# Optimization experiments

Hardware: AMD Instinct MI355X
Metric: run time of the kernel (lower is better)

## Reference

```python
import jax, jax.numpy as jnp
import numpy as np
from jax import lax

B, H, V, L = 128, 256, 130, 100  # batch, hidden_size, vocab per stream, decode length


def _gru(x, h, wih, whh, bih, bhh):
    # torch.nn.GRUCell math
    gi = x @ wih.T + bih
    gh = h @ whh.T + bhh
    ir, iz, inn = jnp.split(gi, 3, axis=-1)
    hr, hz, hn = jnp.split(gh, 3, axis=-1)
    r = jax.nn.sigmoid(ir + hr)
    u = jax.nn.sigmoid(iz + hz)
    n = jnp.tanh(inn + r * hn)
    return (1.0 - u) * n + u * h


def _forward(z, gru1_wih, gru1_whh, gru1_bih, gru1_bhh,
             gru2_wih, gru2_whh, gru2_bih, gru2_bhh,
             ctx_wih, ctx_whh, ctx_bih, ctx_bhh,
             out_w, out_b, hid_w, hid_b, emb, length):
    b = z.shape[0]
    hidden = jnp.tanh(z @ hid_w.T + hid_b)                      # [B,H]
    h3 = jnp.broadcast_to(hidden[None], (3, b, hidden.shape[-1]))
    note0 = jnp.broadcast_to(emb[:, 0][:, None, :], (3, b, emb.shape[-1]))  # embed index 0
    vgru = jax.vmap(_gru)  # over the 3 parallel streams

    def step(carry, _):
        g1h, g2h, context, note = carry
        zb = jnp.broadcast_to(z[None], note.shape)
        g1h = vgru(jnp.concatenate([note, zb], -1), g1h,
                   gru1_wih, gru1_whh, gru1_bih, gru1_bhh)       # [3,B,H]
        unroll = g1h
        logits = []
        for i in range(3):  # fixed structural unroll (3 streams)
            ctx_in = jnp.concatenate([unroll[0], unroll[1], unroll[2]], -1)  # [B,3H]
            context = _gru(ctx_in, context, ctx_wih, ctx_whh, ctx_bih, ctx_bhh)
            h2 = _gru(jnp.concatenate([context, z], -1), g2h[i],
                      gru2_wih[i], gru2_whh[i], gru2_bih[i], gru2_bhh[i])
            g2h = g2h.at[i].set(h2)
            lg = (unroll[i] + h2) @ out_w[i].T + out_b[i]        # [B,V]
            logits.append(lg)
            ni = emb[i][jnp.argmax(lg, axis=-1)]                 # greedy sample -> embed
            note = note.at[i].set(ni)
            # NOTE: original code uses self.gru1[1] here (fixed index 1) -- kept faithful
            unroll = unroll.at[i].set(_gru(jnp.concatenate([ni, z], -1), unroll[i],
                                           gru1_wih[1], gru1_whh[1], gru1_bih[1], gru1_bhh[1]))
        return (g1h, g2h, context, note), jnp.stack(logits)     # [3,B,V]

    _, ys = lax.scan(step, (h3, h3, hidden, note0), None, length=length)
    return jnp.transpose(ys, (1, 2, 0, 3))                      # [3,B,L,V]


def setup_inputs() -> dict:
    key = jax.random.key(0)
    ks = jax.random.split(key, 18)
    s = 0.05
    n = lambda k, shp: jax.random.normal(k, shp, jnp.float32) * s
    return {
        "z": jax.random.normal(ks[0], (B, H), jnp.float32),
        "gru1_wih": n(ks[1], (3, 3 * H, 2 * H)),
        "gru1_whh": n(ks[2], (3, 3 * H, H)),
        "gru1_bih": n(ks[3], (3, 3 * H)),
        "gru1_bhh": n(ks[4], (3, 3 * H)),
        "gru2_wih": n(ks[5], (3, 3 * H, 2 * H)),
        "gru2_whh": n(ks[6], (3, 3 * H, H)),
        "gru2_bih": n(ks[7], (3, 3 * H)),
        "gru2_bhh": n(ks[8], (3, 3 * H)),
        "ctx_wih": n(ks[9], (3 * H, 3 * H)),
        "ctx_whh": n(ks[10], (3 * H, H)),
        "ctx_bih": n(ks[11], (3 * H,)),
        "ctx_bhh": n(ks[12], (3 * H,)),
        "out_w": n(ks[13], (3, V, H)),
        "out_b": n(ks[14], (3, V)),
        "hid_w": n(ks[15], (H, H)),
        "hid_b": n(ks[16], (H,)),
        "emb": n(ks[17], (3, V, H)),
        "length": L,
    }


def reference(z, gru1_wih, gru1_whh, gru1_bih, gru1_bhh,
              gru2_wih, gru2_whh, gru2_bih, gru2_bhh,
              ctx_wih, ctx_whh, ctx_bih, ctx_bhh,
              out_w, out_b, hid_w, hid_b, emb, length):
    return _forward(z, gru1_wih, gru1_whh, gru1_bih, gru1_bhh,
                    gru2_wih, gru2_whh, gru2_bih, gru2_bhh,
                    ctx_wih, ctx_whh, ctx_bih, ctx_bhh,
                    out_w, out_b, hid_w, hid_b, emb, length)
```

## Files before the change

### kernel.cpp

```cpp
#include <hip/hip_runtime.h>
#include <math.h>

#define B 128
#define H 256
#define V 130
#define L 100
#define G3 768
#define BH (B*H)
#define NWG 256
#define NT 1024

#define OFF_FLAGS 0
#define OFF_XRANK 512
#define OFF_CLAIM 640
#define OFF_HID   1024
#define OFF_Z1    (OFF_HID + BH)
#define OFF_Z2    (OFF_Z1 + 3*B*G3)
#define OFF_G1HA  (OFF_Z2 + 3*B*G3)
#define OFF_G1HB  (OFF_G1HA + 3*BH)
#define OFF_H2A   (OFF_G1HB + 3*BH)
#define OFF_H2B   (OFF_H2A + 3*BH)
#define OFF_CTXA  (OFF_H2B + 3*BH)
#define OFF_CTXB  (OFF_CTXA + BH)
#define OFF_U0    (OFF_CTXB + BH)
#define OFF_U1    (OFF_U0 + 3*BH)
#define OFF_NOTE  (OFF_U1 + 3*BH)

typedef float v4f __attribute__((ext_vector_type(4)));

__device__ __forceinline__ float sigmoidf_(float x) { return 1.0f / (1.0f + expf(-x)); }

__device__ __forceinline__ v4f load_coh4(const float* p) {
  v4f v;
  asm volatile("global_load_dwordx4 %0, %1, off sc0 sc1" : "=v"(v) : "v"(p) : "memory");
  return v;
}
__device__ __forceinline__ void store_coh(float* p, float v) {
  asm volatile("global_store_dword %0, %1, off sc0 sc1" :: "v"(p), "v"(v) : "memory");
}
__device__ __forceinline__ void store_coh4(float* p, v4f v) {
  asm volatile("global_store_dwordx4 %0, %1, off sc0 sc1" :: "v"(p), "v"(v) : "memory");
}
__device__ __forceinline__ void waitvm0() {
  asm volatile("s_waitcnt vmcnt(0)" ::: "memory");
}

__device__ __forceinline__ void group_barrier(int* cnt, int grp, int target, int tid) {
  waitvm0();
  __syncthreads();
  if (tid == 0) {
    int* c = cnt + grp * 16;
    __hip_atomic_fetch_add(c, 1, __ATOMIC_RELAXED, __HIP_MEMORY_SCOPE_AGENT);
    while (__hip_atomic_load(c, __ATOMIC_RELAXED, __HIP_MEMORY_SCOPE_AGENT) < target)
      __builtin_amdgcn_s_sleep(1);
  }
  __syncthreads();
}

template <int NCHUNK>
__device__ void gru_phase(
    const float* __restrict__ xc0, const float* __restrict__ xc1,
    const float* __restrict__ xc2, const float* __restrict__ xc3,
    const float* __restrict__ wih, int wih_stride,
    const float* __restrict__ whh,
    const float* __restrict__ zadd,
    const float* __restrict__ bih,
    const float* __restrict__ bhh,
    float* __restrict__ out0, float* __restrict__ out1,
    float* smem, int row0, int col0, int tid)
{
  const float* xc[4] = {xc0, xc1, xc2, xc3};
  v4f stg;
  int sc = 0, srr = 0, sk4 = 0;
  const int nldv = NCHUNK * 256;
  if (tid < nldv) {
    sc  = tid >> 8;
    const int r = tid & 255;
    srr = r >> 6;
    sk4 = (r & 63) << 2;
    stg = load_coh4(xc[sc] + (size_t)(row0 + srr) * H + sk4);
  }
  __syncthreads();
  waitvm0();
  if (tid < nldv) {
    const int sw = (sk4 >> 6) * 65 + (sk4 & 63);
    *reinterpret_cast<v4f*>(smem + sc * 1040 + srr * 260 + sw) = stg;
  }
  __syncthreads();

  const int kq    = tid & 7;
  const int row_l = (tid >> 3) & 3;
  const int col_l = tid >> 5;
  const int col   = col0 + col_l;

  const int klen   = NCHUNK * 32;
  const int kstart = kq * klen;
  const int c      = kstart >> 8;
  const int koff   = kstart & 255;
  const bool is_ih = (c < NCHUNK - 1);

  const float* wb;
  int wstr;
  if (is_ih) { wstr = wih_stride; wb = wih + (size_t)col * wstr + (c * 256 + koff); }
  else       { wstr = 256;        wb = whh + (size_t)col * 256 + koff; }
  const float* wR = wb;
  const float* wZ = wb + (size_t)256 * wstr;
  const float* wN = wb + (size_t)512 * wstr;
  const float* xrow = smem + c * 1040 + row_l * 260;

  float aR = 0.f, aZ = 0.f, aN = 0.f;
#pragma unroll
  for (int kb = 0; kb < (klen == 64 ? 1 : 2); ++kb) {
    const int kof2 = koff + kb * 64;
    const float* xb = xrow + (kof2 >> 6) * 65;
    const float* wRb = wR + kb * 64;
    const float* wZb = wZ + kb * 64;
    const float* wNb = wN + kb * 64;
#pragma unroll
    for (int k = 0; k < 64; k += 4) {
      v4f xv = *reinterpret_cast<const v4f*>(xb + k);
      v4f vR = *reinterpret_cast<const v4f*>(wRb + k);
      v4f vZ = *reinterpret_cast<const v4f*>(wZb + k);
      v4f vN = *reinterpret_cast<const v4f*>(wNb + k);
      aR += xv.x * vR.x; aR += xv.y * vR.y; aR += xv.z * vR.z; aR += xv.w * vR.w;
      aZ += xv.x * vZ.x; aZ += xv.y * vZ.y; aZ += xv.z * vZ.z; aZ += xv.w * vZ.w;
      aN += xv.x * vN.x; aN += xv.y * vN.y; aN += xv.z * vN.z; aN += xv.w * vN.w;
    }
  }
  float aNi = is_ih ? aN : 0.f;
  float aNh = is_ih ? 0.f : aN;
#pragma unroll
  for (int m = 1; m <= 4; m <<= 1) {
    aR  += __shfl_xor(aR, m);
    aZ  += __shfl_xor(aZ, m);
    aNi += __shfl_xor(aNi, m);
    aNh += __shfl_xor(aNh, m);
  }
  if (kq == 0) {
    float bR, bZ, bN;
    if (zadd) {
      const float* zp = zadd + (size_t)(row0 + row_l) * G3;
      bR = zp[col]; bZ = zp[256 + col]; bN = zp[512 + col];
    } else {
      bR = bih[col]; bZ = bih[256 + col]; bN = bih[512 + col];
    }
    const float hR = bhh[col], hZ = bhh[256 + col], hN = bhh[512 + col];
    const float hold = smem[(NCHUNK - 1) * 1040 + row_l * 260 + (col >> 6) * 65 + (col & 63)];
    const float rg = sigmoidf_(aR + bR + hR);
    const float ug = sigmoidf_(aZ + bZ + hZ);
    const float ng = tanhf(aNi + bN + rg * (aNh + hN));
    const float hnew = (1.f - ug) * ng + ug * hold;
    const size_t o = (size_t)(row0 + row_l) * H + col;
    store_coh(out0 + o, hnew);
    if (out1) store_coh(out1 + o, hnew);
  }
}

__device__ void out_phase(
    const float* __restrict__ u0i, const float* __restrict__ h2i,
    const float* __restrict__ ow, const float* __restrict__ ob,
    const float* __restrict__ embi,
    float* __restrict__ note_i, float* __restrict__ outp,
    float* smem, int* sidx, int row, bool active, int tid)
{
  if (!active) return;
  v4f a4, b4;
  if (tid < 64) {
    a4 = load_coh4(u0i + (size_t)row * H + tid * 4);
    b4 = load_coh4(h2i + (size_t)row * H + tid * 4);
  }
  __syncthreads();
  if (tid < 64) {
    waitvm0();
    *reinterpret_cast<v4f*>(smem + tid * 4) = a4 + b4;
  }
  __syncthreads();

  const int v = tid >> 2, kq = tid & 3;
  if (v < V) {
    const float* wrow = ow + (size_t)v * H + kq * 64;
    const float* xr = smem + kq * 64;
    float acc = 0.f;
#pragma unroll
    for (int k = 0; k < 64; k += 4) {
      v4f xv = *reinterpret_cast<const v4f*>(xr + k);
      v4f wv = *reinterpret_cast<const v4f*>(wrow + k);
      acc += xv.x * wv.x; acc += xv.y * wv.y; acc += xv.z * wv.z; acc += xv.w * wv.w;
    }
    acc += __shfl_xor(acc, 1);
    acc += __shfl_xor(acc, 2);
    if (kq == 0) {
      acc += ob[v];
      store_coh(outp + v, acc);
      smem[256 + v] = acc;
    }
  }
  __syncthreads();
  if (tid < 64) {
    float* vals = smem + 256;
    float bv = vals[tid]; int bi = tid;
    float c1 = vals[64 + tid];
    if (c1 > bv) { bv = c1; bi = 64 + tid; }
    if (tid < 2) { float c2 = vals[128 + tid]; if (c2 > bv) { bv = c2; bi = 128 + tid; } }
#pragma unroll
    for (int off = 32; off; off >>= 1) {
      float ov = __shfl_down(bv, off);
      int oi = __shfl_down(bi, off);
      if (ov > bv || (ov == bv && oi < bi)) { bv = ov; bi = oi; }
    }
    if (tid == 0) *sidx = bi;
  }
  __syncthreads();
  const int idx = *sidx;
  if (tid < 64) {
    v4f e = *reinterpret_cast<const v4f*>(embi + (size_t)idx * H + tid * 4);
    store_coh4(note_i + (size_t)row * H + tid * 4, e);
  }
}

__global__ __launch_bounds__(NT, 4) void decoder_persistent(
    const float* __restrict__ g1wih, const float* __restrict__ g1whh,
    const float* __restrict__ g1bhh,
    const float* __restrict__ g2wih, const float* __restrict__ g2whh,
    const float* __restrict__ g2bhh,
    const float* __restrict__ cwih, const float* __restrict__ cwhh,
    const float* __restrict__ cbih, const float* __restrict__ cbhh,
    const float* __restrict__ outw, const float* __restrict__ outb,
    const float* __restrict__ emb,
    float* __restrict__ out, float* __restrict__ wsf)
{
  __shared__ float smem[20608];
  __shared__ int sidx;
  __shared__ int s_tile;
  int* cnt   = reinterpret_cast<int*>(wsf) + OFF_FLAGS;
  int* xrank = reinterpret_cast<int*>(wsf) + OFF_XRANK;
  int* claim = reinterpret_cast<int*>(wsf) + OFF_CLAIM;
  float* Z1   = wsf + OFF_Z1;
  float* Z2   = wsf + OFF_Z2;
  float* g1h[2] = {wsf + OFF_G1HA, wsf + OFF_G1HB};
  float* h2b[2] = {wsf + OFF_H2A,  wsf + OFF_H2B};
  float* ctx[2] = {wsf + OFF_CTXA, wsf + OFF_CTXB};
  float* U0   = wsf + OFF_U0;
  float* U1   = wsf + OFF_U1;
  float* note = wsf + OFF_NOTE;

  const int tid = threadIdx.x;

  if (tid == 0) {
    int xcc;
    asm("s_getreg_b32 %0, hwreg(20, 0, 32)" : "=s"(xcc));
    xcc &= 7;
    int rk = __hip_atomic_fetch_add(xrank + xcc * 16, 1,
                                    __ATOMIC_RELAXED, __HIP_MEMORY_SCOPE_AGENT);
    int tile = (rk < 32) ? (xcc * 32 + rk) : ((int)blockIdx.x & 255);
    for (;;) {
      if (atomicCAS(claim + tile, 0, 1) == 0) break;
      tile = (tile + 1) & 255;
    }
    s_tile = tile;
  }
  __syncthreads();
  const int tile = s_tile;
  const int xs = tile >> 5;
  const int g  = tile & 31;
  const int col0 = xs * 32;
  const int row0 = g * 4;
  const bool oact = (xs < 4);
  const int orow = row0 + xs;
  int ep = 0;

  for (int t = 0; t < L; ++t) {
    const int rbk = t & 1, wbk = (t + 1) & 1;
    for (int s = 0; s < 3; ++s) {
      gru_phase<2>(note + (size_t)s * BH, g1h[rbk] + (size_t)s * BH, nullptr, nullptr,
                   g1wih + (size_t)s * G3 * 512, 512, g1whh + (size_t)s * G3 * H,
                   Z1 + (size_t)s * B * G3, nullptr, g1bhh + (size_t)s * G3,
                   g1h[wbk] + (size_t)s * BH, U0 + (size_t)s * BH,
                   smem, row0, col0, tid);
    }
    group_barrier(cnt, g, (++ep) * 8, tid);
    for (int i = 0; i < 3; ++i) {
      const int j = 3 * t + i;
      const float* us0 = (0 < i ? U1 : U0) + 0 * BH;
      const float* us1 = (1 < i ? U1 : U0) + 1 * BH;
      const float* us2 = (2 < i ? U1 : U0) + 2 * BH;
      gru_phase<4>(us0, us1, us2, ctx[j & 1],
                   cwih, G3, cwhh,
                   nullptr, cbih, cbhh,
                   ctx[(j + 1) & 1], nullptr,
                   smem, row0, col0, tid);
      group_barrier(cnt, g, (++ep) * 8, tid);
      gru_phase<2>(ctx[(j + 1) & 1], h2b[rbk] + (size_t)i * BH, nullptr, nullptr,
                   g2wih + (size_t)i * G3 * 512, 512, g2whh + (size_t)i * G3 * H,
                   Z2 + (size_t)i * B * G3, nullptr, g2bhh + (size_t)i * G3,
                   h2b[wbk] + (size_t)i * BH, nullptr,
                   smem, row0, col0, tid);
      group_barrier(cnt, g, (++ep) * 8, tid);
      out_phase(U0 + (size_t)i * BH, h2b[wbk] + (size_t)i * BH,
                outw + (size_t)i * V * H, outb + (size_t)i * V, emb + (size_t)i * V * H,
                note + (size_t)i * BH,
                out + (size_t)i * B * L * V + (size_t)orow * L * V + (size_t)t * V,
                smem, &sidx, orow, oact, tid);
      group_barrier(cnt, g, (++ep) * 8, tid);
      gru_phase<2>(note + (size_t)i * BH, U0 + (size_t)i * BH, nullptr, nullptr,
                   g1wih + (size_t)1 * G3 * 512, 512, g1whh + (size_t)1 * G3 * H,
                   Z1 + (size_t)1 * B * G3, nullptr, g1bhh + (size_t)1 * G3,
                   U1 + (size_t)i * BH, nullptr,
                   smem, row0, col0, tid);
      group_barrier(cnt, g, (++ep) * 8, tid);
    }
  }
}

__global__ __launch_bounds__(256) void hid_kernel(
    const float* __restrict__ z, const float* __restrict__ hw,
    const float* __restrict__ hb, float* __restrict__ hidden)
{
  __shared__ float xs[32][260];
  const int tid = threadIdx.x;
  const int r = tid & 31, hc = tid >> 5;
  const int row0 = blockIdx.y * 32;
  const int col = blockIdx.x * 8 + hc;
  for (int jj = tid; jj < 32 * 64; jj += 256) {
    const int rr = jj >> 6, k4 = (jj & 63) << 2;
    *reinterpret_cast<float4*>(&xs[rr][k4]) =
        *reinterpret_cast<const float4*>(z + (size_t)(row0 + rr) * H + k4);
  }
  __syncthreads();
  float acc = 0.f;
  const float* wrow = hw + (size_t)col * H;
#pragma unroll 8
  for (int k = 0; k < 256; k += 4) {
    const float4 xv = *reinterpret_cast<const float4*>(&xs[r][k]);
    const float4 wv = *reinterpret_cast<const float4*>(wrow + k);
    acc += xv.x * wv.x; acc += xv.y * wv.y; acc += xv.z * wv.z; acc += xv.w * wv.w;
  }
  hidden[(size_t)(row0 + r) * H + col] = tanhf(acc + hb[col]);
}

__global__ __launch_bounds__(256) void zpre_kernel(
    const float* __restrict__ z, const float* __restrict__ wih,
    const float* __restrict__ bih, float* __restrict__ zout)
{
  __shared__ float xs[32][260];
  const int tid = threadIdx.x;
  const int r = tid & 31, hc = tid >> 5;
  const int row0 = blockIdx.y * 32;
  const int gr = blockIdx.x * 8 + hc;
  const int s = gr / G3;
  const int gg = gr - s * G3;
  for (int jj = tid; jj < 32 * 64; jj += 256) {
    const int rr = jj >> 6, k4 = (jj & 63) << 2;
    *reinterpret_cast<float4*>(&xs[rr][k4]) =
        *reinterpret_cast<const float4*>(z + (size_t)(row0 + rr) * H + k4);
  }
  __syncthreads();
  float acc = 0.f;
  const float* wrow = wih + (size_t)gr * 512 + 256;
#pragma unroll 8
  for (int k = 0; k < 256; k += 4) {
    const float4 xv = *reinterpret_cast<const float4*>(&xs[r][k]);
    const float4 wv = *reinterpret_cast<const float4*>(wrow + k);
    acc += xv.x * wv.x; acc += xv.y * wv.y; acc += xv.z * wv.z; acc += xv.w * wv.w;
  }
  zout[((size_t)(s * B + row0 + r)) * G3 + gg] = acc + bih[gr];
}

__global__ __launch_bounds__(256) void init_copy(
    const float* __restrict__ hidden, float* __restrict__ g1h0,
    float* __restrict__ h20, float* __restrict__ ctx0)
{
  const int e = blockIdx.x * 256 + threadIdx.x;
  const float v = hidden[e];
  ctx0[e] = v;
  for (int s = 0; s < 3; ++s) {
    g1h0[(size_t)s * BH + e] = v;
    h20[(size_t)s * BH + e] = v;
  }
}

__global__ __launch_bounds__(256) void init_note(
    const float* __restrict__ emb, float* __restrict__ note)
{
  const int e = blockIdx.x * 256 + threadIdx.x;
  const int s = e / BH;
  const int c = e & (H - 1);
  note[e] = emb[(size_t)s * V * H + c];
}

__global__ void zero_flags(int* flags) { flags[threadIdx.x] = 0; }

extern "C" void kernel_launch(void* const* d_in, const int* in_sizes, int n_in,
                              void* d_out, int out_size, void* d_ws, size_t ws_size,
                              hipStream_t stream) {
  const float* z     = (const float*)d_in[0];
  const float* g1wih = (const float*)d_in[1];
  const float* g1whh = (const float*)d_in[2];
  const float* g1bih = (const float*)d_in[3];
  const float* g1bhh = (const float*)d_in[4];
  const float* g2wih = (const float*)d_in[5];
  const float* g2whh = (const float*)d_in[6];
  const float* g2bih = (const float*)d_in[7];
  const float* g2bhh = (const float*)d_in[8];
  const float* cwih  = (const float*)d_in[9];
  const float* cwhh  = (const float*)d_in[10];
  const float* cbih  = (const float*)d_in[11];
  const float* cbhh  = (const float*)d_in[12];
  const float* outw  = (const float*)d_in[13];
  const float* outb  = (const float*)d_in[14];
  const float* hidw  = (const float*)d_in[15];
  const float* hidb  = (const float*)d_in[16];
  const float* emb   = (const float*)d_in[17];
  float* out = (float*)d_out;
  float* wsf = (float*)d_ws;
  int* flags = (int*)d_ws;

  const dim3 blk(256);
  hid_kernel<<<dim3(32, 4), blk, 0, stream>>>(z, hidw, hidb, wsf + OFF_HID);
  zpre_kernel<<<dim3(288, 4), blk, 0, stream>>>(z, g1wih, g1bih, wsf + OFF_Z1);
  zpre_kernel<<<dim3(288, 4), blk, 0, stream>>>(z, g2wih, g2bih, wsf + OFF_Z2);
  init_copy<<<128, blk, 0, stream>>>(wsf + OFF_HID, wsf + OFF_G1HA,
                                     wsf + OFF_H2A, wsf + OFF_CTXA);
  init_note<<<384, blk, 0, stream>>>(emb, wsf + OFF_NOTE);
  zero_flags<<<1, 1024, 0, stream>>>(flags);

  decoder_persistent<<<NWG, NT, 0, stream>>>(
      g1wih, g1whh, g1bhh, g2wih, g2whh, g2bhh,
      cwih, cwhh, cbih, cbhh, outw, outb, emb, out, wsf);
}
```

Before: 36.85 ms.

## Place each barrier group within one XCD and relax coherence scope

Rewrites the tile mapping so that the 8 workgroups sharing a row group (and its group barrier) all sit on the same XCD, each taking a column slice. Global loads and stores for exchanged state drop sc1 and keep only sc0. Both changes aim to keep synchronization and data exchange inside the local L2 and avoid cross-die coherence traffic. The claim-based fallback is removed and launch bounds are relaxed. This assumes exactly 32 workgroups land on each XCD; if that does not hold, tiles can collide and sc0-only accesses may read stale data.

```diff
diff --git a/kernel.cpp b/kernel.cpp
--- a/kernel.cpp
+++ b/kernel.cpp
@@ -12,7 +12,6 @@
 
 #define OFF_FLAGS 0
 #define OFF_XRANK 512
-#define OFF_CLAIM 640
 #define OFF_HID   1024
 #define OFF_Z1    (OFF_HID + BH)
 #define OFF_Z2    (OFF_Z1 + 3*B*G3)
@@ -32,14 +31,14 @@
 
 __device__ __forceinline__ v4f load_coh4(const float* p) {
   v4f v;
-  asm volatile("global_load_dwordx4 %0, %1, off sc0 sc1" : "=v"(v) : "v"(p) : "memory");
+  asm volatile("global_load_dwordx4 %0, %1, off sc0" : "=v"(v) : "v"(p) : "memory");
   return v;
 }
 __device__ __forceinline__ void store_coh(float* p, float v) {
-  asm volatile("global_store_dword %0, %1, off sc0 sc1" :: "v"(p), "v"(v) : "memory");
+  asm volatile("global_store_dword %0, %1, off sc0" :: "v"(p), "v"(v) : "memory");
 }
 __device__ __forceinline__ void store_coh4(float* p, v4f v) {
-  asm volatile("global_store_dwordx4 %0, %1, off sc0 sc1" :: "v"(p), "v"(v) : "memory");
+  asm volatile("global_store_dwordx4 %0, %1, off sc0" :: "v"(p), "v"(v) : "memory");
 }
 __device__ __forceinline__ void waitvm0() {
   asm volatile("s_waitcnt vmcnt(0)" ::: "memory");
@@ -218,7 +217,7 @@
   }
 }
 
-__global__ __launch_bounds__(NT, 4) void decoder_persistent(
+__global__ __launch_bounds__(NT) void decoder_persistent(
     const float* __restrict__ g1wih, const float* __restrict__ g1whh,
     const float* __restrict__ g1bhh,
     const float* __restrict__ g2wih, const float* __restrict__ g2whh,
@@ -234,7 +233,6 @@
   __shared__ int s_tile;
   int* cnt   = reinterpret_cast<int*>(wsf) + OFF_FLAGS;
   int* xrank = reinterpret_cast<int*>(wsf) + OFF_XRANK;
-  int* claim = reinterpret_cast<int*>(wsf) + OFF_CLAIM;
   float* Z1   = wsf + OFF_Z1;
   float* Z2   = wsf + OFF_Z2;
   float* g1h[2] = {wsf + OFF_G1HA, wsf + OFF_G1HB};
@@ -251,22 +249,19 @@
     asm("s_getreg_b32 %0, hwreg(20, 0, 32)" : "=s"(xcc));
     xcc &= 7;
     int rk = __hip_atomic_fetch_add(xrank + xcc * 16, 1,
-                                    __ATOMIC_RELAXED, __HIP_MEMORY_SCOPE_AGENT);
-    int tile = (rk < 32) ? (xcc * 32 + rk) : ((int)blockIdx.x & 255);
-    for (;;) {
-      if (atomicCAS(claim + tile, 0, 1) == 0) break;
-      tile = (tile + 1) & 255;
-    }
-    s_tile = tile;
-  }
-  __syncthreads();
-  const int tile = s_tile;
-  const int xs = tile >> 5;
-  const int g  = tile & 31;
-  const int col0 = xs * 32;
+                                    __ATOMIC_RELAXED, __HIP_MEMORY_SCOPE_AGENT) & 31;
+    s_tile = xcc * 32 + rk;
+  }
+  __syncthreads();
+  const int tile  = s_tile;
+  const int xcc   = tile >> 5;
+  const int rank  = tile & 31;
+  const int g     = xcc * 4 + (rank >> 3);
+  const int slice = rank & 7;
+  const int col0 = slice * 32;
   const int row0 = g * 4;
-  const bool oact = (xs < 4);
-  const int orow = row0 + xs;
+  const bool oact = (slice < 4);
+  const int orow = row0 + slice;
   int ep = 0;
 
   for (int t = 0; t < L; ++t) {
```

New measurement: 37.20 ms. No clear change (+1.0%).

## Repartition persistent decoder into 16-row groups with LDS-resident ctx and output weights

Applied to the files above, without the earlier changes.

Changes the persistent kernel's work split from 4-row by 32-column tiles in 32 groups of 8 blocks to 16-row by 8-column tiles in 8 groups of 32 blocks. Each block now keeps its slice of the context input weights and the output projection weights in shared memory for the whole decode, so they are not reloaded from global memory every step. The output/argmax phase is split in two: logits are computed in a distributed way into a workspace buffer, and the argmax is fused into the following unroll GRU phase. This drops the XCC-aware tile claiming. In exchange, each barrier now waits on 32 blocks, and the kernel uses much more shared memory (~160KB), which limits occupancy.

```diff
diff --git a/kernel.cpp b/kernel.cpp
--- a/kernel.cpp
+++ b/kernel.cpp
@@ -11,9 +11,7 @@
 #define NT 1024
 
 #define OFF_FLAGS 0
-#define OFF_XRANK 512
-#define OFF_CLAIM 640
-#define OFF_HID   1024
+#define OFF_HID   512
 #define OFF_Z1    (OFF_HID + BH)
 #define OFF_Z2    (OFF_Z1 + 3*B*G3)
 #define OFF_G1HA  (OFF_Z2 + 3*B*G3)
@@ -25,6 +23,13 @@
 #define OFF_U0    (OFF_CTXB + BH)
 #define OFF_U1    (OFF_U0 + 3*BH)
 #define OFF_NOTE  (OFF_U1 + 3*BH)
+#define OFF_LOG   (OFF_NOTE + 3*BH)
+
+#define LW_CTX 0
+#define LW_OUT 19008
+#define LX     23328
+#define LSIDX  39968
+#define S_TOT  39984
 
 typedef float v4f __attribute__((ext_vector_type(4)));
 
@@ -35,6 +40,11 @@
   asm volatile("global_load_dwordx4 %0, %1, off sc0 sc1" : "=v"(v) : "v"(p) : "memory");
   return v;
 }
+__device__ __forceinline__ float load_coh(const float* p) {
+  float v;
+  asm volatile("global_load_dword %0, %1, off sc0 sc1" : "=v"(v) : "v"(p) : "memory");
+  return v;
+}
 __device__ __forceinline__ void store_coh(float* p, float v) {
   asm volatile("global_store_dword %0, %1, off sc0 sc1" :: "v"(p), "v"(v) : "memory");
 }
@@ -45,11 +55,20 @@
   asm volatile("s_waitcnt vmcnt(0)" ::: "memory");
 }
 
-__device__ __forceinline__ void group_barrier(int* cnt, int grp, int target, int tid) {
+__device__ __forceinline__ void red8(float& a, float& b, float& c, float& d) {
+#pragma unroll
+  for (int m = 1; m <= 4; m <<= 1) {
+    a += __shfl_xor(a, m);
+    b += __shfl_xor(b, m);
+    c += __shfl_xor(c, m);
+    d += __shfl_xor(d, m);
+  }
+}
+
+__device__ __forceinline__ void group_barrier(int* c, int target, int tid) {
   waitvm0();
   __syncthreads();
   if (tid == 0) {
-    int* c = cnt + grp * 16;
     __hip_atomic_fetch_add(c, 1, __ATOMIC_RELAXED, __HIP_MEMORY_SCOPE_AGENT);
     while (__hip_atomic_load(c, __ATOMIC_RELAXED, __HIP_MEMORY_SCOPE_AGENT) < target)
       __builtin_amdgcn_s_sleep(1);
@@ -57,168 +76,212 @@
   __syncthreads();
 }
 
-template <int NCHUNK>
-__device__ void gru_phase(
-    const float* __restrict__ xc0, const float* __restrict__ xc1,
-    const float* __restrict__ xc2, const float* __restrict__ xc3,
-    const float* __restrict__ wih, int wih_stride,
-    const float* __restrict__ whh,
-    const float* __restrict__ zadd,
-    const float* __restrict__ bih,
-    const float* __restrict__ bhh,
-    float* __restrict__ out0, float* __restrict__ out1,
-    float* smem, int row0, int col0, int tid)
-{
-  const float* xc[4] = {xc0, xc1, xc2, xc3};
-  v4f stg;
-  int sc = 0, srr = 0, sk4 = 0;
-  const int nldv = NCHUNK * 256;
-  if (tid < nldv) {
-    sc  = tid >> 8;
-    const int r = tid & 255;
-    srr = r >> 6;
-    sk4 = (r & 63) << 2;
-    stg = load_coh4(xc[sc] + (size_t)(row0 + srr) * H + sk4);
-  }
-  __syncthreads();
-  waitvm0();
-  if (tid < nldv) {
-    const int sw = (sk4 >> 6) * 65 + (sk4 & 63);
-    *reinterpret_cast<v4f*>(smem + sc * 1040 + srr * 260 + sw) = stg;
-  }
-  __syncthreads();
-
-  const int kq    = tid & 7;
-  const int row_l = (tid >> 3) & 3;
-  const int col_l = tid >> 5;
-  const int col   = col0 + col_l;
-
-  const int klen   = NCHUNK * 32;
-  const int kstart = kq * klen;
-  const int c      = kstart >> 8;
-  const int koff   = kstart & 255;
-  const bool is_ih = (c < NCHUNK - 1);
-
-  const float* wb;
-  int wstr;
-  if (is_ih) { wstr = wih_stride; wb = wih + (size_t)col * wstr + (c * 256 + koff); }
-  else       { wstr = 256;        wb = whh + (size_t)col * 256 + koff; }
-  const float* wR = wb;
-  const float* wZ = wb + (size_t)256 * wstr;
-  const float* wN = wb + (size_t)512 * wstr;
-  const float* xrow = smem + c * 1040 + row_l * 260;
-
+__device__ __forceinline__ void gru_compute(
+    float* smem, const float* __restrict__ wih, const float* __restrict__ whh,
+    const float* __restrict__ zadd, const float* __restrict__ bhh,
+    float* out0, float* out1, int row0, int col0, int tid)
+{
+  float* xb = smem + LX;
+  const int kq = tid & 7, row_l = (tid >> 3) & 15;
+  const int col = col0 + (tid >> 7);
+  const int c = kq >> 2, koff = (kq & 3) << 6;
+  const float* xs = xb + row_l * 1040 + c * 260 + (kq & 3) * 65;
+  const float *wR, *wZ, *wN;
+  if (c == 0) {
+    wR = wih + (size_t)col * 512 + koff;
+    wZ = wih + (size_t)(256 + col) * 512 + koff;
+    wN = wih + (size_t)(512 + col) * 512 + koff;
+  } else {
+    wR = whh + (size_t)col * 256 + koff;
+    wZ = whh + (size_t)(256 + col) * 256 + koff;
+    wN = whh + (size_t)(512 + col) * 256 + koff;
+  }
   float aR = 0.f, aZ = 0.f, aN = 0.f;
 #pragma unroll
-  for (int kb = 0; kb < (klen == 64 ? 1 : 2); ++kb) {
-    const int kof2 = koff + kb * 64;
-    const float* xb = xrow + (kof2 >> 6) * 65;
+  for (int j = 0; j < 64; j += 4) {
+    v4f xv = *reinterpret_cast<const v4f*>(xs + j);
+    v4f vR = *reinterpret_cast<const v4f*>(wR + j);
+    v4f vZ = *reinterpret_cast<const v4f*>(wZ + j);
+    v4f vN = *reinterpret_cast<const v4f*>(wN + j);
+    aR += xv.x * vR.x; aR += xv.y * vR.y; aR += xv.z * vR.z; aR += xv.w * vR.w;
+    aZ += xv.x * vZ.x; aZ += xv.y * vZ.y; aZ += xv.z * vZ.z; aZ += xv.w * vZ.w;
+    aN += xv.x * vN.x; aN += xv.y * vN.y; aN += xv.z * vN.z; aN += xv.w * vN.w;
+  }
+  float aNi = (c == 0) ? aN : 0.f;
+  float aNh = (c == 0) ? 0.f : aN;
+  red8(aR, aZ, aNi, aNh);
+  if (kq == 0) {
+    const float* zp = zadd + (size_t)(row0 + row_l) * G3;
+    const float hold = xb[row_l * 1040 + 260 + (col >> 6) * 65 + (col & 63)];
+    const float r2 = sigmoidf_(aR + zp[col] + bhh[col]);
+    const float u2 = sigmoidf_(aZ + zp[256 + col] + bhh[256 + col]);
+    const float n2 = tanhf(aNi + zp[512 + col] + r2 * (aNh + bhh[512 + col]));
+    const float hnew = (1.f - u2) * n2 + u2 * hold;
+    const size_t o = (size_t)(row0 + row_l) * H + col;
+    store_coh(out0 + o, hnew);
+    if (out1) store_coh(out1 + o, hnew);
+  }
+}
+
+__device__ void gru_g(const float* x0, const float* x1,
+    const float* __restrict__ wih, const float* __restrict__ whh,
+    const float* __restrict__ zadd, const float* __restrict__ bhh,
+    float* out0, float* out1, float* smem, int row0, int col0, int tid)
+{
+  float* xb = smem + LX;
+  const int rr = tid >> 6, k4 = (tid & 63) << 2;
+  v4f s0 = load_coh4(x0 + (size_t)(row0 + rr) * H + k4);
+  v4f s1 = load_coh4(x1 + (size_t)(row0 + rr) * H + k4);
+  __syncthreads();
+  waitvm0();
+  const int xo = (k4 >> 6) * 65 + (k4 & 63);
+  *reinterpret_cast<v4f*>(xb + rr * 1040 + xo) = s0;
+  *reinterpret_cast<v4f*>(xb + rr * 1040 + 260 + xo) = s1;
+  __syncthreads();
+  gru_compute(smem, wih, whh, zadd, bhh, out0, out1, row0, col0, tid);
+}
+
+__device__ void ctx_phase(const float* u0p, const float* u1p, const float* u2p,
+    const float* cop, const float* __restrict__ cwhh,
+    const float* __restrict__ cbih, const float* __restrict__ cbhh,
+    float* outc, float* smem, int row0, int col0, int tid)
+{
+  float* xb = smem + LX;
+  const int rr = tid >> 6, k4 = (tid & 63) << 2;
+  const float* xc[4] = {u0p, u1p, u2p, cop};
+  v4f stg[4];
+#pragma unroll
+  for (int c = 0; c < 4; ++c)
+    stg[c] = load_coh4(xc[c] + (size_t)(row0 + rr) * H + k4);
+  __syncthreads();
+  waitvm0();
+  const int xo = (k4 >> 6) * 65 + (k4 & 63);
+#pragma unroll
+  for (int c = 0; c < 4; ++c)
+    *reinterpret_cast<v4f*>(xb + rr * 1040 + c * 260 + xo) = stg[c];
+  __syncthreads();
+
+  const int kq = tid & 7, row_l = (tid >> 3) & 15;
+  const int col_l = tid >> 7;
+  const int col = col0 + col_l;
+  const int c = kq >> 1, koff = (kq & 1) * 128;
+  const float *wR, *wZ, *wN;
+  if (kq < 6) {
+    const float* base = smem + LW_CTX + (size_t)(col_l * 3) * 792 + kq * 132;
+    wR = base; wZ = base + 792; wN = base + 2 * 792;
+  } else {
+    const int hoff = (kq - 6) * 128;
+    wR = cwhh + (size_t)col * 256 + hoff;
+    wZ = cwhh + (size_t)(256 + col) * 256 + hoff;
+    wN = cwhh + (size_t)(512 + col) * 256 + hoff;
+  }
+  float aR = 0.f, aZ = 0.f, aN = 0.f;
+#pragma unroll
+  for (int kb = 0; kb < 2; ++kb) {
+    const float* xs = xb + row_l * 1040 + c * 260 + ((koff + kb * 64) >> 6) * 65;
     const float* wRb = wR + kb * 64;
     const float* wZb = wZ + kb * 64;
     const float* wNb = wN + kb * 64;
 #pragma unroll
-    for (int k = 0; k < 64; k += 4) {
-      v4f xv = *reinterpret_cast<const v4f*>(xb + k);
-      v4f vR = *reinterpret_cast<const v4f*>(wRb + k);
-      v4f vZ = *reinterpret_cast<const v4f*>(wZb + k);
-      v4f vN = *reinterpret_cast<const v4f*>(wNb + k);
+    for (int j = 0; j < 64; j += 4) {
+      v4f xv = *reinterpret_cast<const v4f*>(xs + j);
+      v4f vR = *reinterpret_cast<const v4f*>(wRb + j);
+      v4f vZ = *reinterpret_cast<const v4f*>(wZb + j);
+      v4f vN = *reinterpret_cast<const v4f*>(wNb + j);
       aR += xv.x * vR.x; aR += xv.y * vR.y; aR += xv.z * vR.z; aR += xv.w * vR.w;
       aZ += xv.x * vZ.x; aZ += xv.y * vZ.y; aZ += xv.z * vZ.z; aZ += xv.w * vZ.w;
       aN += xv.x * vN.x; aN += xv.y * vN.y; aN += xv.z * vN.z; aN += xv.w * vN.w;
     }
   }
-  float aNi = is_ih ? aN : 0.f;
-  float aNh = is_ih ? 0.f : aN;
-#pragma unroll
-  for (int m = 1; m <= 4; m <<= 1) {
-    aR  += __shfl_xor(aR, m);
-    aZ  += __shfl_xor(aZ, m);
-    aNi += __shfl_xor(aNi, m);
-    aNh += __shfl_xor(aNh, m);
-  }
+  float aNi = (kq < 6) ? aN : 0.f;
+  float aNh = (kq < 6) ? 0.f : aN;
+  red8(aR, aZ, aNi, aNh);
   if (kq == 0) {
-    float bR, bZ, bN;
-    if (zadd) {
-      const float* zp = zadd + (size_t)(row0 + row_l) * G3;
-      bR = zp[col]; bZ = zp[256 + col]; bN = zp[512 + col];
-    } else {
-      bR = bih[col]; bZ = bih[256 + col]; bN = bih[512 + col];
-    }
-    const float hR = bhh[col], hZ = bhh[256 + col], hN = bhh[512 + col];
-    const float hold = smem[(NCHUNK - 1) * 1040 + row_l * 260 + (col >> 6) * 65 + (col & 63)];
-    const float rg = sigmoidf_(aR + bR + hR);
-    const float ug = sigmoidf_(aZ + bZ + hZ);
-    const float ng = tanhf(aNi + bN + rg * (aNh + hN));
-    const float hnew = (1.f - ug) * ng + ug * hold;
-    const size_t o = (size_t)(row0 + row_l) * H + col;
-    store_coh(out0 + o, hnew);
-    if (out1) store_coh(out1 + o, hnew);
-  }
-}
-
-__device__ void out_phase(
-    const float* __restrict__ u0i, const float* __restrict__ h2i,
-    const float* __restrict__ ow, const float* __restrict__ ob,
-    const float* __restrict__ embi,
-    float* __restrict__ note_i, float* __restrict__ outp,
-    float* smem, int* sidx, int row, bool active, int tid)
-{
-  if (!active) return;
-  v4f a4, b4;
-  if (tid < 64) {
-    a4 = load_coh4(u0i + (size_t)row * H + tid * 4);
-    b4 = load_coh4(h2i + (size_t)row * H + tid * 4);
-  }
-  __syncthreads();
-  if (tid < 64) {
-    waitvm0();
-    *reinterpret_cast<v4f*>(smem + tid * 4) = a4 + b4;
-  }
-  __syncthreads();
-
-  const int v = tid >> 2, kq = tid & 3;
-  if (v < V) {
-    const float* wrow = ow + (size_t)v * H + kq * 64;
-    const float* xr = smem + kq * 64;
+    const float hold = xb[row_l * 1040 + 3 * 260 + (col >> 6) * 65 + (col & 63)];
+    const float r2 = sigmoidf_(aR + cbih[col] + cbhh[col]);
+    const float u2 = sigmoidf_(aZ + cbih[256 + col] + cbhh[256 + col]);
+    const float n2 = tanhf(aNi + cbih[512 + col] + r2 * (aNh + cbhh[512 + col]));
+    store_coh(outc + (size_t)(row0 + row_l) * H + col, (1.f - u2) * n2 + u2 * hold);
+  }
+}
+
+__device__ void logits_phase(const float* u0i, const float* h2i,
+    const float* __restrict__ ob, float* logits_ws, float* outp_d,
+    float* smem, int row0, int rank, int i3, int tid)
+{
+  float* xb = smem + LX;
+  const int rr = tid >> 6, k4 = (tid & 63) << 2;
+  v4f a4 = load_coh4(u0i + (size_t)(row0 + rr) * H + k4);
+  v4f b4 = load_coh4(h2i + (size_t)(row0 + rr) * H + k4);
+  __syncthreads();
+  waitvm0();
+  const int xo = (k4 >> 6) * 65 + (k4 & 63);
+  *reinterpret_cast<v4f*>(xb + rr * 1040 + xo) = a4 + b4;
+  __syncthreads();
+
+  const int kq = tid & 7, row = (tid >> 3) & 15, vs = tid >> 7;
+  const int v = rank * 5 + vs;
+  if (vs < 5 && v < V) {
+    const float* xs = xb + row * 1040 + ((kq * 32) >> 6) * 65 + ((kq * 32) & 63);
+    const float* wp = smem + LW_OUT + (size_t)((i3 * 5 + vs) * 8 + kq) * 36;
     float acc = 0.f;
 #pragma unroll
-    for (int k = 0; k < 64; k += 4) {
-      v4f xv = *reinterpret_cast<const v4f*>(xr + k);
-      v4f wv = *reinterpret_cast<const v4f*>(wrow + k);
+    for (int j = 0; j < 32; j += 4) {
+      v4f xv = *reinterpret_cast<const v4f*>(xs + j);
+      v4f wv = *reinterpret_cast<const v4f*>(wp + j);
       acc += xv.x * wv.x; acc += xv.y * wv.y; acc += xv.z * wv.z; acc += xv.w * wv.w;
     }
     acc += __shfl_xor(acc, 1);
     acc += __shfl_xor(acc, 2);
+    acc += __shfl_xor(acc, 4);
     if (kq == 0) {
       acc += ob[v];
-      store_coh(outp + v, acc);
-      smem[256 + v] = acc;
+      store_coh(logits_ws + (size_t)(row0 + row) * 144 + v, acc);
+      store_coh(outp_d + (size_t)row * (L * V) + v, acc);
     }
   }
-  __syncthreads();
-  if (tid < 64) {
-    float* vals = smem + 256;
-    float bv = vals[tid]; int bi = tid;
-    float c1 = vals[64 + tid];
-    if (c1 > bv) { bv = c1; bi = 64 + tid; }
-    if (tid < 2) { float c2 = vals[128 + tid]; if (c2 > bv) { bv = c2; bi = 128 + tid; } }
-#pragma unroll
-    for (int off = 32; off; off >>= 1) {
-      float ov = __shfl_down(bv, off);
-      int oi = __shfl_down(bi, off);
-      if (ov > bv || (ov == bv && oi < bi)) { bv = ov; bi = oi; }
-    }
-    if (tid == 0) *sidx = bi;
-  }
-  __syncthreads();
-  const int idx = *sidx;
-  if (tid < 64) {
-    v4f e = *reinterpret_cast<const v4f*>(embi + (size_t)idx * H + tid * 4);
-    store_coh4(note_i + (size_t)row * H + tid * 4, e);
-  }
-}
-
-__global__ __launch_bounds__(NT, 4) void decoder_persistent(
+}
+
+__device__ void unroll_phase(const float* logits_ws, const float* __restrict__ embi,
+    const float* u0i, const float* __restrict__ w1ih, const float* __restrict__ w1hh,
+    const float* __restrict__ zadd1, const float* __restrict__ bhh1,
+    float* note_i, float* out_u1, float* smem, int row0, int col0, int tid)
+{
+  float* xb = smem + LX;
+  int* sidx = (int*)(smem + LSIDX);
+  const int w = tid >> 6, l = tid & 63;
+  const float* lr = logits_ws + (size_t)(row0 + w) * 144;
+  float c0 = load_coh(lr + l);
+  float c1 = load_coh(lr + 64 + l);
+  float c2 = -INFINITY;
+  if (l < 2) c2 = load_coh(lr + 128 + l);
+  waitvm0();
+  float bv = c0; int bi = l;
+  if (c1 > bv) { bv = c1; bi = 64 + l; }
+  if (c2 > bv) { bv = c2; bi = 128 + l; }
+#pragma unroll
+  for (int off = 32; off; off >>= 1) {
+    const float ov = __shfl_down(bv, off);
+    const int   oi = __shfl_down(bi, off);
+    if (ov > bv || (ov == bv && oi < bi)) { bv = ov; bi = oi; }
+  }
+  if (l == 0) sidx[w] = bi;
+  __syncthreads();
+
+  const int rr = tid >> 6, k4 = (tid & 63) << 2;
+  const int idx = sidx[rr];
+  v4f e4 = *reinterpret_cast<const v4f*>(embi + (size_t)idx * H + k4);
+  v4f u4 = load_coh4(u0i + (size_t)(row0 + rr) * H + k4);
+  waitvm0();
+  const int xo = (k4 >> 6) * 65 + (k4 & 63);
+  *reinterpret_cast<v4f*>(xb + rr * 1040 + xo) = e4;
+  *reinterpret_cast<v4f*>(xb + rr * 1040 + 260 + xo) = u4;
+  store_coh4(note_i + (size_t)(row0 + rr) * H + k4, e4);
+  __syncthreads();
+  gru_compute(smem, w1ih, w1hh, zadd1, bhh1, out_u1, nullptr, row0, col0, tid);
+}
+
+__global__ __launch_bounds__(NT) void decoder_persistent(
     const float* __restrict__ g1wih, const float* __restrict__ g1whh,
     const float* __restrict__ g1bhh,
     const float* __restrict__ g2wih, const float* __restrict__ g2whh,
@@ -229,12 +292,8 @@
     const float* __restrict__ emb,
     float* __restrict__ out, float* __restrict__ wsf)
 {
-  __shared__ float smem[20608];
-  __shared__ int sidx;
-  __shared__ int s_tile;
-  int* cnt   = reinterpret_cast<int*>(wsf) + OFF_FLAGS;
-  int* xrank = reinterpret_cast<int*>(wsf) + OFF_XRANK;
-  int* claim = reinterpret_cast<int*>(wsf) + OFF_CLAIM;
+  __shared__ float smem[S_TOT];
+  int* flags = reinterpret_cast<int*>(wsf) + OFF_FLAGS;
   float* Z1   = wsf + OFF_Z1;
   float* Z2   = wsf + OFF_Z2;
   float* g1h[2] = {wsf + OFF_G1HA, wsf + OFF_G1HB};
@@ -243,71 +302,70 @@
   float* U0   = wsf + OFF_U0;
   float* U1   = wsf + OFF_U1;
   float* note = wsf + OFF_NOTE;
+  float* LOGW = wsf + OFF_LOG;
 
   const int tid = threadIdx.x;
-
-  if (tid == 0) {
-    int xcc;
-    asm("s_getreg_b32 %0, hwreg(20, 0, 32)" : "=s"(xcc));
-    xcc &= 7;
-    int rk = __hip_atomic_fetch_add(xrank + xcc * 16, 1,
-                                    __ATOMIC_RELAXED, __HIP_MEMORY_SCOPE_AGENT);
-    int tile = (rk < 32) ? (xcc * 32 + rk) : ((int)blockIdx.x & 255);
-    for (;;) {
-      if (atomicCAS(claim + tile, 0, 1) == 0) break;
-      tile = (tile + 1) & 255;
-    }
-    s_tile = tile;
-  }
-  __syncthreads();
-  const int tile = s_tile;
-  const int xs = tile >> 5;
-  const int g  = tile & 31;
-  const int col0 = xs * 32;
-  const int row0 = g * 4;
-  const bool oact = (xs < 4);
-  const int orow = row0 + xs;
+  const int g    = blockIdx.x >> 5;
+  const int rank = blockIdx.x & 31;
+  const int row0 = g * 16;
+  const int col0 = rank * 8;
+  int* cnt = flags + g * 64;
   int ep = 0;
+
+  for (int i = tid; i < 24 * 768; i += NT) {
+    const int cg = i / 768, rem = i - cg * 768;
+    const int kq = rem >> 7, j = rem & 127;
+    const int colg = col0 + cg / 3, gg = cg % 3;
+    smem[LW_CTX + cg * 792 + kq * 132 + j] =
+        cwih[(size_t)(gg * 256 + colg) * 768 + kq * 128 + j];
+  }
+  for (int i = tid; i < 3 * 5 * 8 * 32; i += NT) {
+    const int j = i & 31;
+    const int kq = (i >> 5) & 7;
+    const int vs = (i >> 8) % 5;
+    const int i3 = i / 1280;
+    const int v = rank * 5 + vs;
+    if (v < V)
+      smem[LW_OUT + (size_t)((i3 * 5 + vs) * 8 + kq) * 36 + j] =
+          outw[(size_t)i3 * V * H + (size_t)v * H + kq * 32 + j];
+  }
+  __syncthreads();
 
   for (int t = 0; t < L; ++t) {
     const int rbk = t & 1, wbk = (t + 1) & 1;
-    for (int s = 0; s < 3; ++s) {
-      gru_phase<2>(note + (size_t)s * BH, g1h[rbk] + (size_t)s * BH, nullptr, nullptr,
-                   g1wih + (size_t)s * G3 * 512, 512, g1whh + (size_t)s * G3 * H,
-                   Z1 + (size_t)s * B * G3, nullptr, g1bhh + (size_t)s * G3,
-                   g1h[wbk] + (size_t)s * BH, U0 + (size_t)s * BH,
+    gru_g(note, g1h[rbk], g1wih, g1whh, Z1, g1bhh,
+          g1h[wbk], U0, smem, row0, col0, tid);
+    gru_g(note + BH, g1h[rbk] + BH, g1wih + (size_t)G3 * 512,
+          g1whh + (size_t)G3 * 256, Z1 + (size_t)B * G3, g1bhh + G3,
+          g1h[wbk] + BH, U0 + BH, smem, row0, col0, tid);
+    gru_g(note + 2 * BH, g1h[rbk] + 2 * BH, g1wih + (size_t)2 * G3 * 512,
+          g1whh + (size_t)2 * G3 * 256, Z1 + (size_t)2 * B * G3, g1bhh + 2 * G3,
+          g1h[wbk] + 2 * BH, U0 + 2 * BH, smem, row0, col0, tid);
+    group_barrier(cnt, (++ep) * 32, tid);
+    for (int i = 0; i < 3; ++i) {
+      const int jj = 3 * t + i;
+      const float* us0 = (0 < i ? U1 : U0);
+      const float* us1 = (1 < i ? U1 : U0) + BH;
+      const float* us2 = U0 + 2 * BH;
+      ctx_phase(us0, us1, us2, ctx[jj & 1], cwhh, cbih, cbhh,
+                ctx[(jj + 1) & 1], smem, row0, col0, tid);
+      group_barrier(cnt, (++ep) * 32, tid);
+      gru_g(ctx[(jj + 1) & 1], h2b[rbk] + (size_t)i * BH,
+            g2wih + (size_t)i * G3 * 512, g2whh + (size_t)i * G3 * 256,
+            Z2 + (size_t)i * B * G3, g2bhh + (size_t)i * G3,
+            h2b[wbk] + (size_t)i * BH, nullptr, smem, row0, col0, tid);
+      group_barrier(cnt, (++ep) * 32, tid);
+      logits_phase(U0 + (size_t)i * BH, h2b[wbk] + (size_t)i * BH,
+                   outb + (size_t)i * V, LOGW,
+                   out + ((size_t)(i * B + row0) * L + t) * V,
+                   smem, row0, rank, i, tid);
+      group_barrier(cnt, (++ep) * 32, tid);
+      unroll_phase(LOGW, emb + (size_t)i * V * H, U0 + (size_t)i * BH,
+                   g1wih + (size_t)G3 * 512, g1whh + (size_t)G3 * 256,
+                   Z1 + (size_t)B * G3, g1bhh + G3,
+                   note + (size_t)i * BH, U1 + (size_t)i * BH,
                    smem, row0, col0, tid);
-    }
-    group_barrier(cnt, g, (++ep) * 8, tid);
-    for (int i = 0; i < 3; ++i) {
-      const int j = 3 * t + i;
-      const float* us0 = (0 < i ? U1 : U0) + 0 * BH;
-      const float* us1 = (1 < i ? U1 : U0) + 1 * BH;
-      const float* us2 = (2 < i ? U1 : U0) + 2 * BH;
-      gru_phase<4>(us0, us1, us2, ctx[j & 1],
-                   cwih, G3, cwhh,
-                   nullptr, cbih, cbhh,
-                   ctx[(j + 1) & 1], nullptr,
-                   smem, row0, col0, tid);
-      group_barrier(cnt, g, (++ep) * 8, tid);
-      gru_phase<2>(ctx[(j + 1) & 1], h2b[rbk] + (size_t)i * BH, nullptr, nullptr,
-                   g2wih + (size_t)i * G3 * 512, 512, g2whh + (size_t)i * G3 * H,
-                   Z2 + (size_t)i * B * G3, nullptr, g2bhh + (size_t)i * G3,
-                   h2b[wbk] + (size_t)i * BH, nullptr,
-                   smem, row0, col0, tid);
-      group_barrier(cnt, g, (++ep) * 8, tid);
-      out_phase(U0 + (size_t)i * BH, h2b[wbk] + (size_t)i * BH,
-                outw + (size_t)i * V * H, outb + (size_t)i * V, emb + (size_t)i * V * H,
-                note + (size_t)i * BH,
-                out + (size_t)i * B * L * V + (size_t)orow * L * V + (size_t)t * V,
-                smem, &sidx, orow, oact, tid);
-      group_barrier(cnt, g, (++ep) * 8, tid);
-      gru_phase<2>(note + (size_t)i * BH, U0 + (size_t)i * BH, nullptr, nullptr,
-                   g1wih + (size_t)1 * G3 * 512, 512, g1whh + (size_t)1 * G3 * H,
-                   Z1 + (size_t)1 * B * G3, nullptr, g1bhh + (size_t)1 * G3,
-                   U1 + (size_t)i * BH, nullptr,
-                   smem, row0, col0, tid);
-      group_barrier(cnt, g, (++ep) * 8, tid);
+      group_barrier(cnt, (++ep) * 32, tid);
     }
   }
 }
@@ -422,7 +480,7 @@
   init_copy<<<128, blk, 0, stream>>>(wsf + OFF_HID, wsf + OFF_G1HA,
                                      wsf + OFF_H2A, wsf + OFF_CTXA);
   init_note<<<384, blk, 0, stream>>>(emb, wsf + OFF_NOTE);
-  zero_flags<<<1, 1024, 0, stream>>>(flags);
+  zero_flags<<<1, 512, 0, stream>>>(flags);
 
   decoder_persistent<<<NWG, NT, 0, stream>>>(
       g1wih, g1whh, g1bhh, g2wih, g2whh, g2bhh,
```

After: 33.08 ms, median of 2. 1.11x faster.
